# Performance work log

Hardware: AMD Instinct MI355X
Metric: run time of the kernel (lower is better)

The kernel has to match this reference:

```python
import jax, jax.numpy as jnp
import numpy as np

B, S, D = 1, 2048, 2048
H, KV, HD = 16, 8, 128
GROUP = H // KV
INTER = 6144
L = 2
VOCAB = 32000
EPS = 1e-6
THETA = 10000.0


def _rope_tables(seq_len, head_dim, theta):
    inv_freq = 1.0 / theta ** (np.arange(0, head_dim, 2, dtype=np.float32) / head_dim)
    pos = np.arange(seq_len, dtype=np.float32)
    ang = pos[:, None] * inv_freq[None, :]
    ang = np.concatenate([ang, ang], axis=1)  # [S, HD]
    return jnp.asarray(np.cos(ang)), jnp.asarray(np.sin(ang))


def setup_inputs() -> dict:
    key = jax.random.key(0)
    ks = jax.random.split(key, 16)
    sd = 0.02
    inp = {}
    inp['input_ids'] = jax.random.randint(ks[0], (B, S), 0, VOCAB, dtype=jnp.int32)
    inp['mask'] = jnp.triu(jnp.ones((S, S), dtype=bool), k=1)  # True = masked (future)
    cos, sin = _rope_tables(S, HD, THETA)
    inp['cos'], inp['sin'] = cos, sin
    inp['embed'] = jax.random.normal(ks[1], (VOCAB, D), jnp.float32) * sd
    # torch Linear convention: weight [out, in], y = x @ W.T
    inp['q_w'] = jax.random.normal(ks[2], (L, H * HD, D), jnp.float32) * sd
    inp['k_w'] = jax.random.normal(ks[3], (L, KV * HD, D), jnp.float32) * sd
    inp['v_w'] = jax.random.normal(ks[4], (L, KV * HD, D), jnp.float32) * sd
    inp['o_w'] = jax.random.normal(ks[5], (L, D, H * HD), jnp.float32) * sd
    inp['qn_scale'] = jnp.ones((L, HD), jnp.float32)
    inp['kn_scale'] = jnp.ones((L, HD), jnp.float32)
    inp['ln1_scale'] = jnp.ones((L, D), jnp.float32)
    inp['ln2_scale'] = jnp.ones((L, D), jnp.float32)
    inp['gate_w'] = jax.random.normal(ks[6], (L, INTER, D), jnp.float32) * sd
    inp['up_w'] = jax.random.normal(ks[7], (L, INTER, D), jnp.float32) * sd
    inp['down_w'] = jax.random.normal(ks[8], (L, D, INTER), jnp.float32) * sd
    return inp


def rms_norm(x, scale, eps=EPS):
    xf = x.astype(jnp.float32)
    var = jnp.mean(xf * xf, axis=-1, keepdims=True)
    return (xf * jax.lax.rsqrt(var + eps) * scale).astype(x.dtype)


def apply_rope(x, cos, sin):
    # x: [B, heads, S, HD]
    s = x.shape[2]
    hd = x.shape[-1]
    x1, x2 = x[..., : hd // 2], x[..., hd // 2:]
    rotated = jnp.concatenate([-x2, x1], axis=-1)
    return x * cos[None, None, :s] + rotated * sin[None, None, :s]


def decoder_layer(h, p, mask, cos, sin):
    (q_w, k_w, v_w, o_w, qn, kn, ln1, ln2, gate_w, up_w, down_w) = p
    b, s, _ = h.shape
    x = rms_norm(h, ln1)
    q = (x @ q_w.T).reshape(b, s, H, HD).transpose(0, 2, 1, 3)   # [B,H,S,HD]
    k = (x @ k_w.T).reshape(b, s, KV, HD).transpose(0, 2, 1, 3)  # [B,KV,S,HD]
    v = (x @ v_w.T).reshape(b, s, KV, HD).transpose(0, 2, 1, 3)
    q = rms_norm(q, qn)
    k = rms_norm(k, kn)
    q = apply_rope(q, cos, sin)
    k = apply_rope(k, cos, sin)
    kr = jnp.repeat(k, GROUP, axis=1)  # GQA head expansion
    vr = jnp.repeat(v, GROUP, axis=1)
    scores = jnp.einsum('bhqd,bhkd->bhqk', q, kr) / jnp.sqrt(jnp.float32(HD))
    scores = jnp.where(mask[None, None], -jnp.inf, scores)
    attn = jax.nn.softmax(scores, axis=-1)
    ctx = jnp.einsum('bhqk,bhkd->bhqd', attn, vr)
    ctx = ctx.transpose(0, 2, 1, 3).reshape(b, s, H * HD)
    h = h + ctx @ o_w.T
    x = rms_norm(h, ln2)
    mlp = (jax.nn.silu(x @ gate_w.T) * (x @ up_w.T)) @ down_w.T
    return h + mlp


def reference(input_ids, mask, cos, sin, embed, q_w, k_w, v_w, o_w,
              qn_scale, kn_scale, ln1_scale, ln2_scale, gate_w, up_w, down_w):
    h = embed[input_ids]  # [B, S, D]
    params = (q_w, k_w, v_w, o_w, qn_scale, kn_scale, ln1_scale, ln2_scale,
              gate_w, up_w, down_w)

    def body(carry, p):
        return decoder_layer(carry, p, mask, cos, sin), None

    h, _ = jax.lax.scan(body, h, params)
    return h
```

## Files before the change

### kernel.cpp

```cpp
#include <hip/hip_runtime.h>
#include <hip/hip_bf16.h>

static constexpr int SEQ   = 2048;
static constexpr int DM    = 2048;
static constexpr int NHEAD = 16;
static constexpr int NKVH  = 8;
static constexpr int HDIM  = 128;
static constexpr int FFN   = 6144;
static constexpr int NLAYER = 2;
static constexpr float EPSV = 1e-6f;
static constexpr int QKVN  = NHEAD * HDIM + 2 * NKVH * HDIM;

typedef __attribute__((ext_vector_type(8))) short bf16x8;
typedef __attribute__((ext_vector_type(4))) float f32x4;

__device__ __forceinline__ float wave_sum(float v) {
#pragma unroll
    for (int o = 32; o > 0; o >>= 1) v += __shfl_xor(v, o);
    return v;
}

__device__ __forceinline__ void gload16(const void* g, void* l) {
    __builtin_amdgcn_global_load_lds(
        (const __attribute__((address_space(1))) void*)g,
        (__attribute__((address_space(3))) void*)l,
        16, 0, 0);
}

__global__ void cvt_bf16_k(const float* __restrict__ in, __hip_bfloat16* __restrict__ out) {
    const long b = ((long)blockIdx.x * 256 + threadIdx.x) * 8;
    const float4 a0 = *(const float4*)(in + b);
    const float4 a1 = *(const float4*)(in + b + 4);
    union { bf16x8 v; __hip_bfloat16 h[8]; } u;
    u.h[0] = __float2bfloat16(a0.x); u.h[1] = __float2bfloat16(a0.y);
    u.h[2] = __float2bfloat16(a0.z); u.h[3] = __float2bfloat16(a0.w);
    u.h[4] = __float2bfloat16(a1.x); u.h[5] = __float2bfloat16(a1.y);
    u.h[6] = __float2bfloat16(a1.z); u.h[7] = __float2bfloat16(a1.w);
    *(bf16x8*)(out + b) = u.v;
}

__global__ void embed_k(const int* __restrict__ ids, const float* __restrict__ emb,
                        float* __restrict__ h) {
    const int s = blockIdx.x;
    const long src = (long)ids[s] * DM;
    for (int t = threadIdx.x; t < DM; t += 256)
        h[(long)s * DM + t] = emb[src + t];
}

__global__ void rmsnorm_k(const float* __restrict__ in, const float* __restrict__ g,
                          __hip_bfloat16* __restrict__ out) {
    const int row = blockIdx.x;
    const float* r = in + (long)row * DM;
    const int tid = threadIdx.x;
    float v[8];
    float ss = 0.f;
#pragma unroll
    for (int t = 0; t < 8; ++t) { v[t] = r[tid + t * 256]; ss += v[t] * v[t]; }
    ss = wave_sum(ss);
    __shared__ float sp[4];
    if ((tid & 63) == 0) sp[tid >> 6] = ss;
    __syncthreads();
    ss = sp[0] + sp[1] + sp[2] + sp[3];
    const float inv = rsqrtf(ss * (1.f / DM) + EPSV);
    __hip_bfloat16* o_ = out + (long)row * DM;
#pragma unroll
    for (int t = 0; t < 8; ++t) {
        const int j = tid + t * 256;
        o_[j] = __float2bfloat16(v[t] * inv * g[j]);
    }
}

__global__ void rmsnorm_res4_k(const __hip_bfloat16* __restrict__ part, long n,
                               float* __restrict__ h, const float* __restrict__ g,
                               __hip_bfloat16* __restrict__ x) {
    const int row = blockIdx.x;
    const int tid = threadIdx.x;
    const long base = (long)row * DM + tid * 8;
    float v[8];
    *(float4*)&v[0] = *(const float4*)(h + base);
    *(float4*)&v[4] = *(const float4*)(h + base + 4);
#pragma unroll
    for (int z = 0; z < 4; ++z) {
        union { bf16x8 vv; __hip_bfloat16 e[8]; } p;
        p.vv = *(const bf16x8*)(part + (long)z * n + base);
#pragma unroll
        for (int j = 0; j < 8; ++j) v[j] += __bfloat162float(p.e[j]);
    }
    *(float4*)(h + base) = *(float4*)&v[0];
    *(float4*)(h + base + 4) = *(float4*)&v[4];
    float ss = 0.f;
#pragma unroll
    for (int j = 0; j < 8; ++j) ss += v[j] * v[j];
    ss = wave_sum(ss);
    __shared__ float sp[4];
    if ((tid & 63) == 0) sp[tid >> 6] = ss;
    __syncthreads();
    ss = sp[0] + sp[1] + sp[2] + sp[3];
    const float inv = rsqrtf(ss * (1.f / DM) + EPSV);
    const float4 g0 = *(const float4*)(g + tid * 8);
    const float4 g1 = *(const float4*)(g + tid * 8 + 4);
    union { bf16x8 vv; __hip_bfloat16 e[8]; } o;
    o.e[0] = __float2bfloat16(v[0] * inv * g0.x); o.e[1] = __float2bfloat16(v[1] * inv * g0.y);
    o.e[2] = __float2bfloat16(v[2] * inv * g0.z); o.e[3] = __float2bfloat16(v[3] * inv * g0.w);
    o.e[4] = __float2bfloat16(v[4] * inv * g1.x); o.e[5] = __float2bfloat16(v[5] * inv * g1.y);
    o.e[6] = __float2bfloat16(v[6] * inv * g1.z); o.e[7] = __float2bfloat16(v[7] * inv * g1.w);
    *(bf16x8*)(x + base) = o.vv;
}

__global__ void red4res_k(const __hip_bfloat16* __restrict__ p, long n, float* __restrict__ h) {
    const long i = ((long)blockIdx.x * 256 + threadIdx.x) * 8;
    float v[8];
    *(float4*)&v[0] = *(const float4*)(h + i);
    *(float4*)&v[4] = *(const float4*)(h + i + 4);
#pragma unroll
    for (int z = 0; z < 4; ++z) {
        union { bf16x8 vv; __hip_bfloat16 e[8]; } b;
        b.vv = *(const bf16x8*)(p + (long)z * n + i);
#pragma unroll
        for (int j = 0; j < 8; ++j) v[j] += __bfloat162float(b.e[j]);
    }
    *(float4*)(h + i) = *(float4*)&v[0];
    *(float4*)(h + i + 4) = *(float4*)&v[4];
}

__global__ void qknorm_rope_k(const __hip_bfloat16* __restrict__ in, long zStride, int inOff,
                              const float* __restrict__ ns,
                              const float* __restrict__ cosT, const float* __restrict__ sinT,
                              __hip_bfloat16* __restrict__ out, int nheads) {
    const int idx = blockIdx.x * 4 + (threadIdx.x >> 6);
    const int lane = threadIdx.x & 63;
    const int s = idx / nheads;
    const int hh = idx - s * nheads;
    const long base = (long)s * QKVN + inOff + hh * HDIM;
    const float x1 = __bfloat162float(in[base + lane]) + __bfloat162float(in[zStride + base + lane]);
    const float x2 = __bfloat162float(in[base + lane + 64]) + __bfloat162float(in[zStride + base + lane + 64]);
    float ss = wave_sum(x1 * x1 + x2 * x2);
    const float inv = rsqrtf(ss * (1.f / HDIM) + EPSV);
    const float n1 = x1 * inv * ns[lane];
    const float n2 = x2 * inv * ns[lane + 64];
    const float c1 = cosT[s * HDIM + lane],      c2 = cosT[s * HDIM + 64 + lane];
    const float s1 = sinT[s * HDIM + lane],      s2 = sinT[s * HDIM + 64 + lane];
    __hip_bfloat16* w = out + ((long)hh * SEQ + s) * HDIM;
    w[lane]      = __float2bfloat16(n1 * c1 - n2 * s1);
    w[lane + 64] = __float2bfloat16(n2 * c2 + n1 * s2);
}

__global__ void vtrans_k(const __hip_bfloat16* __restrict__ vf, long zStride, int colOff,
                         __hip_bfloat16* __restrict__ vt) {
    __shared__ float tile[64][65];
    const int s0 = blockIdx.x * 64, d0 = blockIdx.y * 64, kv = blockIdx.z;
    const int lane = threadIdx.x & 63, part = threadIdx.x >> 6;
    for (int r = part; r < 64; r += 4) {
        const long idx = (long)(s0 + r) * QKVN + colOff + kv * HDIM + d0 + lane;
        tile[r][lane] = __bfloat162float(vf[idx]) + __bfloat162float(vf[zStride + idx]);
    }
    __syncthreads();
    for (int r = part; r < 64; r += 4)
        vt[((long)kv * HDIM + d0 + r) * SEQ + s0 + lane] = __float2bfloat16(tile[lane][r]);
}

__global__ void silu_red2_k(const __hip_bfloat16* __restrict__ p, long n,
                            __hip_bfloat16* __restrict__ out) {
    const long i = ((long)blockIdx.x * 256 + threadIdx.x) * 8;
    union { bf16x8 v; __hip_bfloat16 e[8]; } g0, g1, u0, u1, o;
    g0.v = *(const bf16x8*)(p + i);
    g1.v = *(const bf16x8*)(p + n + i);
    u0.v = *(const bf16x8*)(p + 2 * n + i);
    u1.v = *(const bf16x8*)(p + 3 * n + i);
#pragma unroll
    for (int j = 0; j < 8; ++j) {
        const float g = __bfloat162float(g0.e[j]) + __bfloat162float(g1.e[j]);
        const float u = __bfloat162float(u0.e[j]) + __bfloat162float(u1.e[j]);
        const float sv = g / (1.f + __expf(-g));
        o.e[j] = __float2bfloat16(sv * u);
    }
    *(bf16x8*)(out + i) = o.v;
}

__global__ __launch_bounds__(256)
void flash_k(const __hip_bfloat16* __restrict__ qb, const __hip_bfloat16* __restrict__ kb,
             const __hip_bfloat16* __restrict__ vt, __hip_bfloat16* __restrict__ ctx) {
    __shared__ __align__(16) char ks[2][16384];
    __shared__ __align__(16) char vs[2][16384];
    __shared__ __align__(16) char ps[4][2048];

    const int tid = threadIdx.x;
    const int lane = tid & 63;
    const int wid = tid >> 6;
    const int l15 = lane & 15;
    const int l4 = lane >> 4;

    const int h = blockIdx.y;
    const int kvh = h >> 1;
    const float scale = 0.0883883476483184405f;

    auto stageK = [&](int buf, int kt) {
        const __hip_bfloat16* kg = kb + ((long)kvh * SEQ + kt * 64) * HDIM;
#pragma unroll
        for (int i = 0; i < 4; ++i) {
            const int c = i * 256 + tid;
            const int r = c >> 4, s = c & 15;
            gload16(kg + (long)r * HDIM + ((s ^ (r & 7)) * 8), ks[buf] + c * 16);
        }
    };
    auto stageV = [&](int buf, int kt) {
        const __hip_bfloat16* vg = vt + (long)kvh * HDIM * SEQ + kt * 64;
#pragma unroll
        for (int i = 0; i < 4; ++i) {
            const int c = i * 256 + tid;
            const int r = c >> 3, s = c & 7;
            gload16(vg + (long)r * SEQ + ((s ^ (r & 7)) * 8), vs[buf] + c * 16);
        }
    };

#pragma unroll
    for (int half = 0; half < 2; ++half) {
        const int x = half ? 31 - blockIdx.x : blockIdx.x;
        const int q0 = x * 64;
        const int nkt = x + 1;

        bf16x8 aq[4];
        {
            const __hip_bfloat16* qg = qb + ((long)h * SEQ + q0 + wid * 16 + l15) * HDIM + l4 * 8;
#pragma unroll
            for (int kk = 0; kk < 4; ++kk) aq[kk] = *(const bf16x8*)(qg + kk * 32);
        }

        float mreg[4], lreg[4];
#pragma unroll
        for (int j = 0; j < 4; ++j) { mreg[j] = -3.0e38f; lreg[j] = 0.f; }
        f32x4 oacc[8];
#pragma unroll
        for (int n = 0; n < 8; ++n) oacc[n] = (f32x4){0.f, 0.f, 0.f, 0.f};

        stageK(0, 0); stageV(0, 0);
        asm volatile("s_waitcnt vmcnt(0)" ::: "memory");
        __builtin_amdgcn_s_barrier();

        for (int kt = 0; kt < nkt; ++kt) {
            const int cur = kt & 1;
            if (kt + 1 < nkt) { stageK(cur ^ 1, kt + 1); stageV(cur ^ 1, kt + 1); }

            f32x4 sac[4];
#pragma unroll
            for (int n = 0; n < 4; ++n) sac[n] = (f32x4){0.f, 0.f, 0.f, 0.f};
            __builtin_amdgcn_s_setprio(1);
#pragma unroll
            for (int kk = 0; kk < 4; ++kk) {
#pragma unroll
                for (int n = 0; n < 4; ++n) {
                    const int r = n * 16 + l15;
                    const bf16x8 bk = *(const bf16x8*)(ks[cur] + r * 256 + (((kk * 4 + l4) ^ (r & 7)) << 4));
                    sac[n] = __builtin_amdgcn_mfma_f32_16x16x32_bf16(aq[kk], bk, sac[n], 0, 0, 0);
                }
            }
            __builtin_amdgcn_s_setprio(0);

            const bool diag = (kt + 1 == nkt);
            float mnj[4], alj[4];
#pragma unroll
            for (int j = 0; j < 4; ++j) {
                float mx = -3.0e38f;
#pragma unroll
                for (int n = 0; n < 4; ++n) {
                    float v = sac[n][j] * scale;
                    if (diag && (n * 16 + l15 > wid * 16 + l4 * 4 + j)) v = -3.0e38f;
                    sac[n][j] = v;
                    mx = fmaxf(mx, v);
                }
#pragma unroll
                for (int o = 1; o < 16; o <<= 1) mx = fmaxf(mx, __shfl_xor(mx, o));
                const float mn = fmaxf(mreg[j], mx);
                mnj[j] = mn;
                alj[j] = __expf(mreg[j] - mn);
                mreg[j] = mn;
            }
#pragma unroll
            for (int j = 0; j < 4; ++j) {
                float rs = 0.f;
#pragma unroll
                for (int n = 0; n < 4; ++n) {
                    const float e = __expf(sac[n][j] - mnj[j]);
                    sac[n][j] = e;
                    rs += e;
                }
#pragma unroll
                for (int o = 1; o < 16; o <<= 1) rs += __shfl_xor(rs, o);
                lreg[j] = lreg[j] * alj[j] + rs;
#pragma unroll
                for (int n2 = 0; n2 < 8; ++n2) oacc[n2][j] *= alj[j];
            }

            char* pw = ps[wid];
#pragma unroll
            for (int n = 0; n < 4; ++n)
#pragma unroll
                for (int j = 0; j < 4; ++j) {
                    const int r = l4 * 4 + j;
                    const int col = n * 16 + l15;
                    *(__hip_bfloat16*)(pw + r * 128 + (((col >> 3) ^ (r & 7)) << 4) + (col & 7) * 2) =
                        __float2bfloat16(sac[n][j]);
                }
            asm volatile("s_waitcnt lgkmcnt(0)" ::: "memory");
            __builtin_amdgcn_sched_barrier(0);
            __builtin_amdgcn_s_setprio(1);
#pragma unroll
            for (int kk = 0; kk < 2; ++kk) {
                const bf16x8 ap = *(const bf16x8*)(pw + l15 * 128 + (((kk * 4 + l4) ^ (l15 & 7)) << 4));
#pragma unroll
                for (int n2 = 0; n2 < 8; ++n2) {
                    const int r = n2 * 16 + l15;
                    const bf16x8 bv = *(const bf16x8*)(vs[cur] + r * 128 + (((kk * 4 + l4) ^ (r & 7)) << 4));
                    oacc[n2] = __builtin_amdgcn_mfma_f32_16x16x32_bf16(ap, bv, oacc[n2], 0, 0, 0);
                }
            }
            __builtin_amdgcn_s_setprio(0);

            asm volatile("s_waitcnt vmcnt(0)" ::: "memory");
            __builtin_amdgcn_s_barrier();
        }

#pragma unroll
        for (int j = 0; j < 4; ++j) {
            const float inv = 1.f / lreg[j];
            const long rowb = (long)(q0 + wid * 16 + l4 * 4 + j) * (NHEAD * HDIM) + h * HDIM;
#pragma unroll
            for (int n2 = 0; n2 < 8; ++n2)
                ctx[rowb + n2 * 16 + l15] = __float2bfloat16(oacc[n2][j] * inv);
        }
    }
}

template <int OUT>
__global__ __launch_bounds__(512, 2)
void g8p(const __hip_bfloat16* __restrict__ A, const __hip_bfloat16* __restrict__ B,
         void* __restrict__ Cv, int kLen, int ldA, int ldB, int ldC,
         long bZStride, long cZStride, int kZStride, int zDiv) {
    __shared__ __align__(16) char sA[2][2][16384];
    __shared__ __align__(16) char sB[2][2][16384];

    const int tid = threadIdx.x;
    const int lane = tid & 63;
    const int wid = tid >> 6;
    const int wr = wid >> 2;
    const int wc = wid & 3;
    const int l15 = lane & 15;
    const int l4 = lane >> 4;

    const int row0 = blockIdx.y * 256;
    const int col0 = blockIdx.x * 256;

    const int z = blockIdx.z;
    B += (long)(z / zDiv) * bZStride;
    const long cOff = (long)z * cZStride;
    const int k0z = (z % zDiv) * kZStride;
    const int nk = kLen / 64;

    f32x4 acc[8][4];
#pragma unroll
    for (int m = 0; m < 8; ++m)
#pragma unroll
        for (int n = 0; n < 4; ++n)
            acc[m][n] = (f32x4){0.f, 0.f, 0.f, 0.f};

    auto stage = [&](int kind, int kt) {
        const int k0 = k0z + kt * 64;
        const __hip_bfloat16* base;
        int ld_;
        char* dst;
        if (kind < 2) { base = A + (long)(row0 + kind * 128) * ldA; ld_ = ldA; dst = sA[kt & 1][kind]; }
        else          { base = B + (long)(col0 + (kind - 2) * 128) * ldB; ld_ = ldB; dst = sB[kt & 1][kind - 2]; }
#pragma unroll
        for (int i = 0; i < 2; ++i) {
            const int c = i * 512 + tid;
            const int r = c >> 3;
            const int s = c & 7;
            gload16(base + (long)r * ld_ + k0 + ((s ^ (r & 7)) * 8), dst + c * 16);
        }
    };

    auto readA = [&](int buf, int p, int mm, int ks) -> bf16x8 {
        const int r = p * 32 + mm * 16 + l15;
        const int q = ks * 4 + l4;
        return *(const bf16x8*)(sA[buf][wr] + r * 128 + ((q ^ (r & 7)) << 4));
    };
    auto readB = [&](int buf, int nn, int ks) -> bf16x8 {
        const int r = (wc & 1) * 64 + nn * 16 + l15;
        const int q = ks * 4 + l4;
        return *(const bf16x8*)(sB[buf][wc >> 1] + r * 128 + ((q ^ (r & 7)) << 4));
    };

    stage(0, 0); stage(1, 0); stage(2, 0); stage(3, 0);
    stage(2, 1); stage(3, 1);
    asm volatile("s_waitcnt vmcnt(4)" ::: "memory");
    __builtin_amdgcn_s_barrier();

    bf16x8 bfrag[4][2];
    for (int t = 0; t < nk; ++t) {
        const int cur = t & 1;
#pragma unroll
        for (int p = 0; p < 4; ++p) {
            bf16x8 a[2][2];
            a[0][0] = readA(cur, p, 0, 0); a[0][1] = readA(cur, p, 0, 1);
            a[1][0] = readA(cur, p, 1, 0); a[1][1] = readA(cur, p, 1, 1);
            if (p == 0) {
#pragma unroll
                for (int n = 0; n < 4; ++n) {
                    bfrag[n][0] = readB(cur, n, 0);
                    bfrag[n][1] = readB(cur, n, 1);
                }
            }
            if (p == 0 && t + 1 < nk) stage(0, t + 1);
            if (p == 1 && t + 1 < nk) stage(1, t + 1);
            if (p == 2 && t + 2 < nk) stage(2, t + 2);
            if (p == 3 && t + 2 < nk) stage(3, t + 2);

            if (p == 0) asm volatile("s_waitcnt lgkmcnt(8)" ::: "memory");
            __builtin_amdgcn_sched_barrier(0);
            if (p == 3) {
                if (t + 2 < nk)      asm volatile("s_waitcnt vmcnt(4)" ::: "memory");
                else if (t + 1 < nk) asm volatile("s_waitcnt vmcnt(0)" ::: "memory");
            }
            __builtin_amdgcn_s_barrier();
            asm volatile("s_waitcnt lgkmcnt(0)" ::: "memory");
            __builtin_amdgcn_sched_barrier(0);

            __builtin_amdgcn_s_setprio(1);
#pragma unroll
            for (int ks = 0; ks < 2; ++ks)
#pragma unroll
                for (int mm = 0; mm < 2; ++mm)
#pragma unroll
                    for (int n = 0; n < 4; ++n)
                        acc[p * 2 + mm][n] = __builtin_amdgcn_mfma_f32_16x16x32_bf16(
                            a[mm][ks], bfrag[n][ks], acc[p * 2 + mm][n], 0, 0, 0);
            __builtin_amdgcn_s_setprio(0);
            __builtin_amdgcn_sched_barrier(0);
            __builtin_amdgcn_s_barrier();
        }
    }

#pragma unroll
    for (int m = 0; m < 8; ++m) {
#pragma unroll
        for (int n = 0; n < 4; ++n) {
            const int rb = row0 + wr * 128 + m * 16 + l4 * 4;
            const int cc = col0 + wc * 64 + n * 16 + l15;
#pragma unroll
            for (int j = 0; j < 4; ++j) {
                const long idx = cOff + (long)(rb + j) * ldC + cc;
                if constexpr (OUT == 0) ((float*)Cv)[idx] = acc[m][n][j];
                else                    ((__hip_bfloat16*)Cv)[idx] = __float2bfloat16(acc[m][n][j]);
            }
        }
    }
}

extern "C" void kernel_launch(void* const* d_in, const int* in_sizes, int n_in,
                              void* d_out, int out_size, void* d_ws, size_t ws_size,
                              hipStream_t stream) {
    const int*   ids  = (const int*)d_in[0];
    const float* cosT = (const float*)d_in[2];
    const float* sinT = (const float*)d_in[3];
    const float* emb  = (const float*)d_in[4];
    const float* q_w  = (const float*)d_in[5];
    const float* k_w  = (const float*)d_in[6];
    const float* v_w  = (const float*)d_in[7];
    const float* o_w  = (const float*)d_in[8];
    const float* qn   = (const float*)d_in[9];
    const float* kn   = (const float*)d_in[10];
    const float* ln1  = (const float*)d_in[11];
    const float* ln2  = (const float*)d_in[12];
    const float* gw   = (const float*)d_in[13];
    const float* uw   = (const float*)d_in[14];
    const float* dw   = (const float*)d_in[15];

    char* W = (char*)d_ws;
    size_t off = 0;
    auto take = [&](size_t nb) { char* p = W + off; off += (nb + 255) & ~(size_t)255; return p; };

    __hip_bfloat16* wqkv = (__hip_bfloat16*) take((size_t)NLAYER * QKVN * DM * 2);
    __hip_bfloat16* wo   = (__hip_bfloat16*) take((size_t)NLAYER * DM * (NHEAD * HDIM) * 2);
    __hip_bfloat16* wgu  = (__hip_bfloat16*) take((size_t)NLAYER * 2 * FFN * DM * 2);
    __hip_bfloat16* wd   = (__hip_bfloat16*) take((size_t)NLAYER * DM * FFN * 2);
    float*          h    = (float*)          take((size_t)SEQ * DM * 4);
    __hip_bfloat16* x    = (__hip_bfloat16*) take((size_t)SEQ * DM * 2);
    __hip_bfloat16* part = (__hip_bfloat16*) take((size_t)4 * SEQ * FFN * 2);
    __hip_bfloat16* qb   = (__hip_bfloat16*) take((size_t)NHEAD * SEQ * HDIM * 2);
    __hip_bfloat16* kb   = (__hip_bfloat16*) take((size_t)NKVH * SEQ * HDIM * 2);
    __hip_bfloat16* vt   = (__hip_bfloat16*) take((size_t)NKVH * HDIM * SEQ * 2);
    __hip_bfloat16* ctx  = (__hip_bfloat16*) take((size_t)SEQ * NHEAD * HDIM * 2);
    __hip_bfloat16* go   = (__hip_bfloat16*) take((size_t)SEQ * FFN * 2);
    if (off > ws_size) return;

    auto cvt = [&](const float* src, __hip_bfloat16* dst, long n) {
        cvt_bf16_k<<<(int)(n / 2048), 256, 0, stream>>>(src, dst);
    };

    for (int l = 0; l < NLAYER; ++l) {
        __hip_bfloat16* base = wqkv + (size_t)l * QKVN * DM;
        cvt(q_w + (size_t)l * (NHEAD * HDIM) * DM, base,                               (long)(NHEAD * HDIM) * DM);
        cvt(k_w + (size_t)l * (NKVH * HDIM) * DM,  base + (size_t)(NHEAD * HDIM) * DM, (long)(NKVH * HDIM) * DM);
        cvt(v_w + (size_t)l * (NKVH * HDIM) * DM,  base + (size_t)(NHEAD * HDIM + NKVH * HDIM) * DM, (long)(NKVH * HDIM) * DM);
        cvt(gw + (size_t)l * FFN * DM, wgu + (size_t)(2 * l)     * FFN * DM, (long)FFN * DM);
        cvt(uw + (size_t)l * FFN * DM, wgu + (size_t)(2 * l + 1) * FFN * DM, (long)FFN * DM);
    }
    cvt(o_w, wo, (long)NLAYER * DM * (NHEAD * HDIM));
    cvt(dw,  wd, (long)NLAYER * DM * FFN);

    embed_k<<<SEQ, 256, 0, stream>>>(ids, emb, h);
    rmsnorm_k<<<SEQ, 256, 0, stream>>>(h, ln1, x);

    const long nQKV = (long)SEQ * QKVN;
    const long nDM  = (long)SEQ * DM;
    const long nFFN = (long)SEQ * FFN;

    for (int l = 0; l < NLAYER; ++l) {
        g8p<1><<<dim3(QKVN / 256, SEQ / 256, 2), 512, 0, stream>>>(
            x, wqkv + (size_t)l * QKVN * DM, part, DM / 2, DM, DM, QKVN,
            0L, nQKV, DM / 2, 2);

        qknorm_rope_k<<<SEQ * NHEAD / 4, 256, 0, stream>>>(
            part, nQKV, 0, qn + l * HDIM, cosT, sinT, qb, NHEAD);
        qknorm_rope_k<<<SEQ * NKVH / 4, 256, 0, stream>>>(
            part, nQKV, NHEAD * HDIM, kn + l * HDIM, cosT, sinT, kb, NKVH);
        vtrans_k<<<dim3(SEQ / 64, HDIM / 64, NKVH), 256, 0, stream>>>(
            part, nQKV, NHEAD * HDIM + NKVH * HDIM, vt);

        flash_k<<<dim3(16, NHEAD), 256, 0, stream>>>(qb, kb, vt, ctx);

        g8p<1><<<dim3(DM / 256, SEQ / 256, 4), 512, 0, stream>>>(
            ctx, wo + (size_t)l * DM * (NHEAD * HDIM), part, (NHEAD * HDIM) / 4,
            NHEAD * HDIM, NHEAD * HDIM, DM, 0L, nDM, (NHEAD * HDIM) / 4, 4);
        rmsnorm_res4_k<<<SEQ, 256, 0, stream>>>(part, nDM, h, ln2 + l * DM, x);

        g8p<1><<<dim3(FFN / 256, SEQ / 256, 4), 512, 0, stream>>>(
            x, wgu + (size_t)(2 * l) * FFN * DM, part, DM / 2, DM, DM, FFN,
            (long)FFN * DM, nFFN, DM / 2, 2);
        silu_red2_k<<<(int)(nFFN / 2048), 256, 0, stream>>>(part, nFFN, go);

        g8p<1><<<dim3(DM / 256, SEQ / 256, 4), 512, 0, stream>>>(
            go, wd + (size_t)l * DM * FFN, part, FFN / 4,
            FFN, FFN, DM, 0L, nDM, FFN / 4, 4);
        if (l + 1 < NLAYER)
            rmsnorm_res4_k<<<SEQ, 256, 0, stream>>>(part, nDM, h, ln1 + (l + 1) * DM, x);
        else
            red4res_k<<<(int)(nDM / 2048), 256, 0, stream>>>(part, nDM, h);
    }

    hipMemcpyAsync(d_out, h, (size_t)out_size * sizeof(float), hipMemcpyDeviceToDevice, stream);
}
```

Baseline: 913.5 us.

## Fuse fp32-to-bf16 weight conversion into GEMM B-operand loading

Drops the separate weight conversion kernels and bf16 weight buffers. The GEMM now reads fp32 weights straight from the original q/k/v, o, gate/up and down arrays into registers, converts them to bf16 and writes them to swizzled LDS, with the QKV segments chosen per column block. This removes one full read and write pass over all weights, but the GEMM now reads twice as many weight bytes, each tile is re-read by every row block and split-K slice, and the B path goes through registers instead of direct global-to-LDS loads. That may raise memory traffic and register pressure in the main loop.

```diff
diff --git a/kernel.cpp b/kernel.cpp
--- a/kernel.cpp
+++ b/kernel.cpp
@@ -25,18 +25,6 @@
         (const __attribute__((address_space(1))) void*)g,
         (__attribute__((address_space(3))) void*)l,
         16, 0, 0);
-}
-
-__global__ void cvt_bf16_k(const float* __restrict__ in, __hip_bfloat16* __restrict__ out) {
-    const long b = ((long)blockIdx.x * 256 + threadIdx.x) * 8;
-    const float4 a0 = *(const float4*)(in + b);
-    const float4 a1 = *(const float4*)(in + b + 4);
-    union { bf16x8 v; __hip_bfloat16 h[8]; } u;
-    u.h[0] = __float2bfloat16(a0.x); u.h[1] = __float2bfloat16(a0.y);
-    u.h[2] = __float2bfloat16(a0.z); u.h[3] = __float2bfloat16(a0.w);
-    u.h[4] = __float2bfloat16(a1.x); u.h[5] = __float2bfloat16(a1.y);
-    u.h[6] = __float2bfloat16(a1.z); u.h[7] = __float2bfloat16(a1.w);
-    *(bf16x8*)(out + b) = u.v;
 }
 
 __global__ void embed_k(const int* __restrict__ ids, const float* __restrict__ emb,
@@ -331,11 +319,12 @@
     }
 }
 
-template <int OUT>
+template <int ZSEL>
 __global__ __launch_bounds__(512, 2)
-void g8p(const __hip_bfloat16* __restrict__ A, const __hip_bfloat16* __restrict__ B,
-         void* __restrict__ Cv, int kLen, int ldA, int ldB, int ldC,
-         long bZStride, long cZStride, int kZStride, int zDiv) {
+void g8p(const __hip_bfloat16* __restrict__ A,
+         const float* __restrict__ Ba, const float* __restrict__ Bb, const float* __restrict__ Bc,
+         __hip_bfloat16* __restrict__ C, int kLen, int ldA, int ldB, int ldC,
+         int seg1, int seg2, long cZStride, int kZStride, int zDiv) {
     __shared__ __align__(16) char sA[2][2][16384];
     __shared__ __align__(16) char sB[2][2][16384];
 
@@ -349,9 +338,17 @@
 
     const int row0 = blockIdx.y * 256;
     const int col0 = blockIdx.x * 256;
-
     const int z = blockIdx.z;
-    B += (long)(z / zDiv) * bZStride;
+
+    const float* B;
+    int colB;
+    if (ZSEL) {
+        B = (z / zDiv) ? Bb : Ba; colB = col0;
+    } else {
+        if (col0 >= seg2)      { B = Bc; colB = col0 - seg2; }
+        else if (col0 >= seg1) { B = Bb; colB = col0 - seg1; }
+        else                   { B = Ba; colB = col0; }
+    }
     const long cOff = (long)z * cZStride;
     const int k0z = (z % zDiv) * kZStride;
     const int nk = kLen / 64;
@@ -363,19 +360,40 @@
         for (int n = 0; n < 4; ++n)
             acc[m][n] = (f32x4){0.f, 0.f, 0.f, 0.f};
 
-    auto stage = [&](int kind, int kt) {
+    auto stageA = [&](int half, int kt) {
+        const __hip_bfloat16* base = A + (long)(row0 + half * 128) * ldA;
+        char* dst = sA[kt & 1][half];
         const int k0 = k0z + kt * 64;
-        const __hip_bfloat16* base;
-        int ld_;
-        char* dst;
-        if (kind < 2) { base = A + (long)(row0 + kind * 128) * ldA; ld_ = ldA; dst = sA[kt & 1][kind]; }
-        else          { base = B + (long)(col0 + (kind - 2) * 128) * ldB; ld_ = ldB; dst = sB[kt & 1][kind - 2]; }
 #pragma unroll
         for (int i = 0; i < 2; ++i) {
             const int c = i * 512 + tid;
-            const int r = c >> 3;
-            const int s = c & 7;
-            gload16(base + (long)r * ld_ + k0 + ((s ^ (r & 7)) * 8), dst + c * 16);
+            const int r = c >> 3, s = c & 7;
+            gload16(base + (long)r * ldA + k0 + ((s ^ (r & 7)) * 8), dst + c * 16);
+        }
+    };
+    auto loadB = [&](float4* rb, int half, int kt) {
+        const int k0 = k0z + kt * 64;
+        const float* base = B + (long)(colB + half * 128) * ldB + k0;
+#pragma unroll
+        for (int i = 0; i < 2; ++i) {
+            const int sidx = i * 512 + tid;
+            const int r = sidx >> 3, q = sidx & 7;
+            const float* p = base + (long)r * ldB + q * 8;
+            rb[i * 2]     = *(const float4*)p;
+            rb[i * 2 + 1] = *(const float4*)(p + 4);
+        }
+    };
+    auto writeB = [&](const float4* rb, int half, int kt) {
+        char* dst = sB[kt & 1][half];
+#pragma unroll
+        for (int i = 0; i < 2; ++i) {
+            const int sidx = i * 512 + tid;
+            const int r = sidx >> 3, q = sidx & 7;
+            union { bf16x8 v; __hip_bfloat16 e[8]; } u;
+            const float* f = (const float*)&rb[i * 2];
+#pragma unroll
+            for (int j = 0; j < 8; ++j) u.e[j] = __float2bfloat16(f[j]);
+            *(bf16x8*)(dst + (r * 8 + (q ^ (r & 7))) * 16) = u.v;
         }
     };
 
@@ -390,9 +408,17 @@
         return *(const bf16x8*)(sB[buf][wc >> 1] + r * 128 + ((q ^ (r & 7)) << 4));
     };
 
-    stage(0, 0); stage(1, 0); stage(2, 0); stage(3, 0);
-    stage(2, 1); stage(3, 1);
+    float4 rb0[4], rb1[4];
+    loadB(rb0, 0, 0);
+    stageA(0, 0); stageA(1, 0);
     asm volatile("s_waitcnt vmcnt(4)" ::: "memory");
+    writeB(rb0, 0, 0);
+    loadB(rb1, 1, 0);
+    asm volatile("s_waitcnt vmcnt(0)" ::: "memory");
+    writeB(rb1, 1, 0);
+    if (nk > 1) { loadB(rb0, 0, 1); loadB(rb1, 1, 1); }
+    asm volatile("s_waitcnt lgkmcnt(0)" ::: "memory");
+    __builtin_amdgcn_sched_barrier(0);
     __builtin_amdgcn_s_barrier();
 
     bf16x8 bfrag[4][2];
@@ -410,15 +436,15 @@
                     bfrag[n][1] = readB(cur, n, 1);
                 }
             }
-            if (p == 0 && t + 1 < nk) stage(0, t + 1);
-            if (p == 1 && t + 1 < nk) stage(1, t + 1);
-            if (p == 2 && t + 2 < nk) stage(2, t + 2);
-            if (p == 3 && t + 2 < nk) stage(3, t + 2);
+            if (p == 0 && t + 1 < nk) { stageA(0, t + 1); writeB(rb0, 0, t + 1); }
+            if (p == 1 && t + 1 < nk) { stageA(1, t + 1); writeB(rb1, 1, t + 1); }
+            if (p == 2 && t + 2 < nk) loadB(rb0, 0, t + 2);
+            if (p == 3 && t + 2 < nk) loadB(rb1, 1, t + 2);
 
             if (p == 0) asm volatile("s_waitcnt lgkmcnt(8)" ::: "memory");
             __builtin_amdgcn_sched_barrier(0);
             if (p == 3) {
-                if (t + 2 < nk)      asm volatile("s_waitcnt vmcnt(4)" ::: "memory");
+                if (t + 2 < nk)      asm volatile("s_waitcnt vmcnt(8)" ::: "memory");
                 else if (t + 1 < nk) asm volatile("s_waitcnt vmcnt(0)" ::: "memory");
             }
             __builtin_amdgcn_s_barrier();
@@ -447,11 +473,8 @@
             const int rb = row0 + wr * 128 + m * 16 + l4 * 4;
             const int cc = col0 + wc * 64 + n * 16 + l15;
 #pragma unroll
-            for (int j = 0; j < 4; ++j) {
-                const long idx = cOff + (long)(rb + j) * ldC + cc;
-                if constexpr (OUT == 0) ((float*)Cv)[idx] = acc[m][n][j];
-                else                    ((__hip_bfloat16*)Cv)[idx] = __float2bfloat16(acc[m][n][j]);
-            }
+            for (int j = 0; j < 4; ++j)
+                C[cOff + (long)(rb + j) * ldC + cc] = __float2bfloat16(acc[m][n][j]);
         }
     }
 }
@@ -479,10 +502,6 @@
     size_t off = 0;
     auto take = [&](size_t nb) { char* p = W + off; off += (nb + 255) & ~(size_t)255; return p; };
 
-    __hip_bfloat16* wqkv = (__hip_bfloat16*) take((size_t)NLAYER * QKVN * DM * 2);
-    __hip_bfloat16* wo   = (__hip_bfloat16*) take((size_t)NLAYER * DM * (NHEAD * HDIM) * 2);
-    __hip_bfloat16* wgu  = (__hip_bfloat16*) take((size_t)NLAYER * 2 * FFN * DM * 2);
-    __hip_bfloat16* wd   = (__hip_bfloat16*) take((size_t)NLAYER * DM * FFN * 2);
     float*          h    = (float*)          take((size_t)SEQ * DM * 4);
     __hip_bfloat16* x    = (__hip_bfloat16*) take((size_t)SEQ * DM * 2);
     __hip_bfloat16* part = (__hip_bfloat16*) take((size_t)4 * SEQ * FFN * 2);
@@ -493,32 +512,26 @@
     __hip_bfloat16* go   = (__hip_bfloat16*) take((size_t)SEQ * FFN * 2);
     if (off > ws_size) return;
 
-    auto cvt = [&](const float* src, __hip_bfloat16* dst, long n) {
-        cvt_bf16_k<<<(int)(n / 2048), 256, 0, stream>>>(src, dst);
-    };
-
-    for (int l = 0; l < NLAYER; ++l) {
-        __hip_bfloat16* base = wqkv + (size_t)l * QKVN * DM;
-        cvt(q_w + (size_t)l * (NHEAD * HDIM) * DM, base,                               (long)(NHEAD * HDIM) * DM);
-        cvt(k_w + (size_t)l * (NKVH * HDIM) * DM,  base + (size_t)(NHEAD * HDIM) * DM, (long)(NKVH * HDIM) * DM);
-        cvt(v_w + (size_t)l * (NKVH * HDIM) * DM,  base + (size_t)(NHEAD * HDIM + NKVH * HDIM) * DM, (long)(NKVH * HDIM) * DM);
-        cvt(gw + (size_t)l * FFN * DM, wgu + (size_t)(2 * l)     * FFN * DM, (long)FFN * DM);
-        cvt(uw + (size_t)l * FFN * DM, wgu + (size_t)(2 * l + 1) * FFN * DM, (long)FFN * DM);
-    }
-    cvt(o_w, wo, (long)NLAYER * DM * (NHEAD * HDIM));
-    cvt(dw,  wd, (long)NLAYER * DM * FFN);
-
     embed_k<<<SEQ, 256, 0, stream>>>(ids, emb, h);
     rmsnorm_k<<<SEQ, 256, 0, stream>>>(h, ln1, x);
 
     const long nQKV = (long)SEQ * QKVN;
     const long nDM  = (long)SEQ * DM;
     const long nFFN = (long)SEQ * FFN;
+    const int BIG = 1 << 30;
 
     for (int l = 0; l < NLAYER; ++l) {
-        g8p<1><<<dim3(QKVN / 256, SEQ / 256, 2), 512, 0, stream>>>(
-            x, wqkv + (size_t)l * QKVN * DM, part, DM / 2, DM, DM, QKVN,
-            0L, nQKV, DM / 2, 2);
+        const float* qwl = q_w + (size_t)l * (NHEAD * HDIM) * DM;
+        const float* kwl = k_w + (size_t)l * (NKVH * HDIM) * DM;
+        const float* vwl = v_w + (size_t)l * (NKVH * HDIM) * DM;
+        const float* owl = o_w + (size_t)l * DM * (NHEAD * HDIM);
+        const float* gwl = gw  + (size_t)l * FFN * DM;
+        const float* uwl = uw  + (size_t)l * FFN * DM;
+        const float* dwl = dw  + (size_t)l * DM * FFN;
+
+        g8p<0><<<dim3(QKVN / 256, SEQ / 256, 2), 512, 0, stream>>>(
+            x, qwl, kwl, vwl, part, DM / 2, DM, DM, QKVN,
+            NHEAD * HDIM, NHEAD * HDIM + NKVH * HDIM, nQKV, DM / 2, 2);
 
         qknorm_rope_k<<<SEQ * NHEAD / 4, 256, 0, stream>>>(
             part, nQKV, 0, qn + l * HDIM, cosT, sinT, qb, NHEAD);
@@ -529,19 +542,19 @@
 
         flash_k<<<dim3(16, NHEAD), 256, 0, stream>>>(qb, kb, vt, ctx);
 
-        g8p<1><<<dim3(DM / 256, SEQ / 256, 4), 512, 0, stream>>>(
-            ctx, wo + (size_t)l * DM * (NHEAD * HDIM), part, (NHEAD * HDIM) / 4,
-            NHEAD * HDIM, NHEAD * HDIM, DM, 0L, nDM, (NHEAD * HDIM) / 4, 4);
+        g8p<0><<<dim3(DM / 256, SEQ / 256, 4), 512, 0, stream>>>(
+            ctx, owl, owl, owl, part, (NHEAD * HDIM) / 4, NHEAD * HDIM, NHEAD * HDIM, DM,
+            BIG, BIG, nDM, (NHEAD * HDIM) / 4, 4);
         rmsnorm_res4_k<<<SEQ, 256, 0, stream>>>(part, nDM, h, ln2 + l * DM, x);
 
         g8p<1><<<dim3(FFN / 256, SEQ / 256, 4), 512, 0, stream>>>(
-            x, wgu + (size_t)(2 * l) * FFN * DM, part, DM / 2, DM, DM, FFN,
-            (long)FFN * DM, nFFN, DM / 2, 2);
+            x, gwl, uwl, uwl, part, DM / 2, DM, DM, FFN,
+            BIG, BIG, nFFN, DM / 2, 2);
         silu_red2_k<<<(int)(nFFN / 2048), 256, 0, stream>>>(part, nFFN, go);
 
-        g8p<1><<<dim3(DM / 256, SEQ / 256, 4), 512, 0, stream>>>(
-            go, wd + (size_t)l * DM * FFN, part, FFN / 4,
-            FFN, FFN, DM, 0L, nDM, FFN / 4, 4);
+        g8p<0><<<dim3(DM / 256, SEQ / 256, 4), 512, 0, stream>>>(
+            go, dwl, dwl, dwl, part, FFN / 4, FFN, FFN, DM,
+            BIG, BIG, nDM, FFN / 4, 4);
         if (l + 1 < NLAYER)
             rmsnorm_res4_k<<<SEQ, 256, 0, stream>>>(part, nDM, h, ln1 + (l + 1) * DM, x);
         else
```

Result: faster. 847.9 us (-7.2%).
